# Kernel optimization log

Hardware: AMD Instinct MI355X
Metric: run time of the kernel (lower is better)

## Reference

```python
import jax, jax.numpy as jnp
import numpy as np

N_NODES = 100000
N_EDGES = 1600000
D_IN = 64
D_OUT = 64
NUM_ETYPE = 2
NEG_SLOPE = 0.2


def setup_inputs() -> dict:
    key = jax.random.key(0)
    ks = jax.random.split(key, 9)
    feat = jax.random.normal(ks[0], (N_NODES, D_IN), dtype=jnp.float32)
    rel = jax.random.uniform(ks[1], (N_EDGES, NUM_ETYPE), dtype=jnp.float32)
    W_self = jax.random.normal(ks[2], (D_OUT, D_IN), dtype=jnp.float32) * 0.1
    b_self = jax.random.normal(ks[3], (D_OUT,), dtype=jnp.float32) * 0.1
    W_neigh = jax.random.normal(ks[4], (D_OUT, D_IN), dtype=jnp.float32) * 0.1
    b_neigh = jax.random.normal(ks[5], (D_OUT,), dtype=jnp.float32) * 0.1
    attn_e = jax.random.normal(ks[6], (NUM_ETYPE, 1), dtype=jnp.float32)
    src = jax.random.randint(ks[7], (N_EDGES,), 0, N_NODES, dtype=jnp.int32)
    dst = jax.random.randint(ks[8], (N_EDGES,), 0, N_NODES, dtype=jnp.int32)
    return {"feat": feat, "rel": rel, "W_self": W_self, "b_self": b_self,
            "W_neigh": W_neigh, "b_neigh": b_neigh, "attn_e": attn_e,
            "src": src, "dst": dst}


def reference(feat, rel, W_self, b_self, W_neigh, b_neigh, attn_e, src, dst):
    n = feat.shape[0]
    # per-edge attention score: [E, num_etype] @ [num_etype, 1] -> [E]
    e = jnp.squeeze(rel @ attn_e, axis=1)
    e = jax.nn.leaky_relu(e, negative_slope=NEG_SLOPE)
    # edge_softmax: segment softmax over edges grouped by destination node
    emax = jax.ops.segment_max(e, dst, num_segments=n)          # [N]
    ex = jnp.exp(e - emax[dst])                                  # [E]
    denom = jax.ops.segment_sum(ex, dst, num_segments=n)        # [N]
    a = ex / denom[dst]                                          # [E]
    # u_mul_e + sum aggregation: neigh[v] = sum_e a_e * feat[src_e]
    m = feat[src] * a[:, None]                                   # [E, D_IN]
    h_neigh = jax.ops.segment_sum(m, dst, num_segments=n)       # [N, D_IN]
    # rst = fc_self(h_self) + fc_neigh(h_neigh)  (torch Linear: x @ W.T + b)
    return feat @ W_self.T + b_self + h_neigh @ W_neigh.T + b_neigh
```

## Files before the change

kernel.cpp:

```cpp
#include <hip/hip_runtime.h>
#include <hip/hip_bf16.h>

#define N_NODES 100000
#define N_EDGES 1600000
#define D 64
#define NEG_SLOPE 0.2f

#define BSHIFT 9
#define BNODES 512
#define NBUCK ((N_NODES + BNODES - 1) >> BSHIFT)
#define BUCKET_CAP 8896
#define P1_EPB 4096
#define P1_T 512
#define P1_IT (P1_EPB / P1_T)
#define GRID_BIN ((N_EDGES + P1_EPB - 1) / P1_EPB)

typedef __attribute__((ext_vector_type(8))) short bf16x8;
typedef __attribute__((ext_vector_type(4))) float f32x4;
#define MFMA16(a, b, c) __builtin_amdgcn_mfma_f32_16x16x32_bf16(a, b, c, 0, 0, 0)

__device__ __forceinline__ short bf16_rne(float f) {
    unsigned u = __float_as_uint(f);
    u += 0x7FFFu + ((u >> 16) & 1u);
    return (short)(u >> 16);
}
__device__ __forceinline__ float bf16_to_f(short h) {
    return __uint_as_float(((unsigned)(unsigned short)h) << 16);
}
__device__ __forceinline__ void cvt8(float4 f0, float4 f1,
                                     bf16x8& hi, bf16x8& lo) {
    float v[8] = {f0.x, f0.y, f0.z, f0.w, f1.x, f1.y, f1.z, f1.w};
    #pragma unroll
    for (int j = 0; j < 8; ++j) {
        short h = bf16_rne(v[j]);
        hi[j] = h;
        lo[j] = bf16_rne(v[j] - bf16_to_f(h));
    }
}

__global__ __launch_bounds__(P1_T) void binning_kernel(
    const float2* __restrict__ rel, const float* __restrict__ attn_e,
    const int* __restrict__ src, const int* __restrict__ dst,
    int* __restrict__ bucket_cursor, uint2* __restrict__ binned,
    const float* __restrict__ W_self, const float* __restrict__ W_neigh,
    const float* __restrict__ b_self, const float* __restrict__ b_neigh,
    bf16x8* __restrict__ wfrag, float* __restrict__ bsum)
{
    __shared__ uint2 staged1[P1_EPB];
    __shared__ uint2 staged2[P1_EPB];
    __shared__ int cnt[NBUCK];
    __shared__ int excl[NBUCK];
    __shared__ int chunkbase[NBUCK];

    int tid = threadIdx.x;

    if (blockIdx.x == GRID_BIN) {
        if (tid < D) bsum[tid] = b_self[tid] + b_neigh[tid];
        for (int c = tid; c < 1024; c += P1_T) {
            int nt = c >> 8;
            int mat = (c >> 7) & 1;
            int s = (c >> 6) & 1;
            int lane = c & 63;
            const float* Wm = mat ? W_neigh : W_self;
            int row = nt * 16 + (lane & 15);
            int koff = s * 32 + (lane >> 4) * 8;
            const float4* p = (const float4*)(Wm + row * D + koff);
            bf16x8 hi, lo;
            cvt8(p[0], p[1], hi, lo);
            int base = (c >> 6) * 128 + (c & 63);
            wfrag[base] = hi;
            wfrag[base + 64] = lo;
        }
        return;
    }

    int e0 = blockIdx.x * P1_EPB;
    int n = min(P1_EPB, N_EDGES - e0);

    for (int b = tid; b < NBUCK; b += P1_T) cnt[b] = 0;
    __syncthreads();

    float a0 = attn_e[0], a1 = attn_e[1];

    int myslot[P1_IT];
    #pragma unroll
    for (int j = 0; j < P1_IT; ++j) {
        int i = tid + j * P1_T;
        if (i < n) {
            int e = e0 + i;
            float2 r = rel[e];
            float sc = r.x * a0 + r.y * a1;
            sc = (sc > 0.f) ? sc : NEG_SLOPE * sc;
            float ev = __expf(sc);
            unsigned u = __float_as_uint(ev) + 0x8000u;
            unsigned wcode = (u >> 16) & 0x7FFFu;
            unsigned s = (unsigned)src[e];
            unsigned d = (unsigned)dst[e];
            staged1[i] = make_uint2((s << 15) | wcode, d);
            myslot[j] = atomicAdd(&cnt[d >> BSHIFT], 1);
        }
    }
    __syncthreads();
    if (tid == 0) {
        int run = 0;
        for (int b = 0; b < NBUCK; ++b) { excl[b] = run; run += cnt[b]; }
    }
    __syncthreads();
    #pragma unroll
    for (int j = 0; j < P1_IT; ++j) {
        int i = tid + j * P1_T;
        if (i < n) {
            uint2 v = staged1[i];
            staged2[excl[v.y >> BSHIFT] + myslot[j]] = v;
        }
    }
    if (tid < NBUCK)
        chunkbase[tid] = atomicAdd(&bucket_cursor[tid], cnt[tid]);
    __syncthreads();
    for (int i = tid; i < n; i += P1_T) {
        uint2 v = staged2[i];
        int b = (int)(v.y >> BSHIFT);
        binned[(size_t)b * BUCKET_CAP + chunkbase[b] + (i - excl[b])] = v;
    }
}

__global__ __launch_bounds__(1024) void csr_kernel(
    const int* __restrict__ bucket_cursor, const uint2* __restrict__ binned,
    int* __restrict__ offsets, unsigned* __restrict__ edata)
{
    __shared__ unsigned vals[BUCKET_CAP];
    __shared__ int hist[BNODES];
    __shared__ int nexcl[BNODES];
    __shared__ int cur[BNODES];
    __shared__ int bc[NBUCK];
    __shared__ int base_sh;

    int b = blockIdx.x;
    int tid = threadIdx.x;

    if (tid < NBUCK) bc[tid] = bucket_cursor[tid];
    if (tid < BNODES) { hist[tid] = 0; cur[tid] = 0; }
    __syncthreads();
    if (tid == 0) {
        int s = 0;
        for (int i = 0; i < b; ++i) s += bc[i];
        base_sh = s;
    }
    __syncthreads();
    int count = bc[b];
    int base = base_sh;
    const uint2* bin = binned + (size_t)b * BUCKET_CAP;

    for (int i = tid; i < count; i += 1024)
        atomicAdd(&hist[bin[i].y & (BNODES - 1)], 1);
    __syncthreads();

    int h = 0;
    if (tid < BNODES) { h = hist[tid]; nexcl[tid] = h; }
    __syncthreads();
    for (int d = 1; d < BNODES; d <<= 1) {
        int u = (tid >= d && tid < BNODES) ? nexcl[tid - d] : 0;
        __syncthreads();
        if (tid < BNODES) nexcl[tid] += u;
        __syncthreads();
    }
    int excl = 0;
    if (tid < BNODES) excl = nexcl[tid] - h;
    __syncthreads();
    if (tid < BNODES) nexcl[tid] = excl;
    __syncthreads();

    int node = (b << BSHIFT) + tid;
    if (tid < BNODES && node < N_NODES) offsets[node] = base + excl;
    if (b == NBUCK - 1 && tid == 0) offsets[N_NODES] = N_EDGES;

    for (int i = tid; i < count; i += 1024) {
        uint2 e = bin[i];
        int d = e.y & (BNODES - 1);
        int t = atomicAdd(&cur[d], 1);
        vals[nexcl[d] + t] = e.x;
    }
    __syncthreads();
    for (int i = tid; i < count; i += 1024)
        edata[base + i] = vals[i];
}

__global__ __launch_bounds__(256) void gemm_fused_kernel(
    const float* __restrict__ feat, const bf16x8* __restrict__ wfrag,
    const float* __restrict__ bsum, float* __restrict__ out,
    __hip_bfloat16* __restrict__ g)
{
    int tid = threadIdx.x;
    int lane = tid & 63;
    int wave = tid >> 6;
    int llo = lane & 15;
    int lhi = lane >> 4;
    int rb = blockIdx.x * 64 + wave * 16;
    if (rb >= N_NODES) return;

    int node = rb + llo;
    bool valid = node < N_NODES;
    int nclamp = valid ? node : N_NODES - 1;
    const float4* fr = (const float4*)(feat + (size_t)nclamp * D);
    bf16x8 fhi[2], flo[2];
    #pragma unroll
    for (int s = 0; s < 2; ++s)
        cvt8(fr[s * 8 + lhi * 2], fr[s * 8 + lhi * 2 + 1], fhi[s], flo[s]);

    const float4* bs4 = (const float4*)bsum;
    unsigned short* g16 = (unsigned short*)g;

    #pragma unroll
    for (int nt = 0; nt < 4; ++nt) {
        int base = nt * 512 + lane;
        bf16x8 wSh0 = wfrag[base];
        bf16x8 wSl0 = wfrag[base + 64];
        bf16x8 wSh1 = wfrag[base + 128];
        bf16x8 wSl1 = wfrag[base + 192];
        bf16x8 wNh0 = wfrag[base + 256];
        bf16x8 wNl0 = wfrag[base + 320];
        bf16x8 wNh1 = wfrag[base + 384];
        bf16x8 wNl1 = wfrag[base + 448];
        f32x4 accS = {0.f, 0.f, 0.f, 0.f};
        f32x4 accN = {0.f, 0.f, 0.f, 0.f};
        accS = MFMA16(wSh0, fhi[0], accS);
        accN = MFMA16(wNh0, fhi[0], accN);
        accS = MFMA16(wSl0, fhi[0], accS);
        accN = MFMA16(wNl0, fhi[0], accN);
        accS = MFMA16(wSh0, flo[0], accS);
        accN = MFMA16(wNh0, flo[0], accN);
        accS = MFMA16(wSh1, fhi[1], accS);
        accN = MFMA16(wNh1, fhi[1], accN);
        accS = MFMA16(wSl1, fhi[1], accS);
        accN = MFMA16(wNl1, fhi[1], accN);
        accS = MFMA16(wSh1, flo[1], accS);
        accN = MFMA16(wNh1, flo[1], accN);

        if (valid) {
            float4 bb = bs4[nt * 4 + lhi];
            float4 o;
            o.x = accS[0] + bb.x;
            o.y = accS[1] + bb.y;
            o.z = accS[2] + bb.z;
            o.w = accS[3] + bb.w;
            *(float4*)(out + (size_t)node * D + nt * 16 + lhi * 4) = o;
            uint2 gp;
            gp.x = (unsigned)(unsigned short)bf16_rne(accN[0])
                 | ((unsigned)(unsigned short)bf16_rne(accN[1]) << 16);
            gp.y = (unsigned)(unsigned short)bf16_rne(accN[2])
                 | ((unsigned)(unsigned short)bf16_rne(accN[3]) << 16);
            *(uint2*)(g16 + (size_t)node * D + nt * 16 + lhi * 4) = gp;
        }
    }
}

__global__ __launch_bounds__(256) void aggregate_kernel(
    const uint* __restrict__ g32, const unsigned* __restrict__ edata,
    const int* __restrict__ offsets, float* __restrict__ out)
{
    int v = blockIdx.x * 4 + (threadIdx.x >> 6);
    int lane = threadIdx.x & 63;
    int q = lane >> 4;
    int t = lane & 15;
    int lo = offsets[v], hi = offsets[v + 1];
    float4 acc = make_float4(0.f, 0.f, 0.f, 0.f);
    float sum = 0.f;

    for (int i = lo; i < hi; i += 16) {
        int e0 = i + q;
        int e1 = i + 4 + q;
        int e2 = i + 8 + q;
        int e3 = i + 12 + q;
        int ec0 = (e0 < hi) ? e0 : hi - 1;
        int ec1 = (e1 < hi) ? e1 : hi - 1;
        int ec2 = (e2 < hi) ? e2 : hi - 1;
        int ec3 = (e3 < hi) ? e3 : hi - 1;
        unsigned p0 = edata[ec0];
        unsigned p1 = edata[ec1];
        unsigned p2 = edata[ec2];
        unsigned p3 = edata[ec3];
        float w0 = (e0 < hi) ? __uint_as_float((p0 & 0x7FFFu) << 16) : 0.f;
        float w1 = (e1 < hi) ? __uint_as_float((p1 & 0x7FFFu) << 16) : 0.f;
        float w2 = (e2 < hi) ? __uint_as_float((p2 & 0x7FFFu) << 16) : 0.f;
        float w3 = (e3 < hi) ? __uint_as_float((p3 & 0x7FFFu) << 16) : 0.f;
        const uint2* r0 = (const uint2*)(g32 + (size_t)(p0 >> 15) * (D / 2));
        const uint2* r1 = (const uint2*)(g32 + (size_t)(p1 >> 15) * (D / 2));
        const uint2* r2 = (const uint2*)(g32 + (size_t)(p2 >> 15) * (D / 2));
        const uint2* r3 = (const uint2*)(g32 + (size_t)(p3 >> 15) * (D / 2));
        uint2 u0 = r0[t];
        uint2 u1 = r1[t];
        uint2 u2 = r2[t];
        uint2 u3 = r3[t];
        acc.x += w0 * __uint_as_float(u0.x << 16);
        acc.y += w0 * __uint_as_float(u0.x & 0xFFFF0000u);
        acc.z += w0 * __uint_as_float(u0.y << 16);
        acc.w += w0 * __uint_as_float(u0.y & 0xFFFF0000u);
        sum += w0;
        acc.x += w1 * __uint_as_float(u1.x << 16);
        acc.y += w1 * __uint_as_float(u1.x & 0xFFFF0000u);
        acc.z += w1 * __uint_as_float(u1.y << 16);
        acc.w += w1 * __uint_as_float(u1.y & 0xFFFF0000u);
        sum += w1;
        acc.x += w2 * __uint_as_float(u2.x << 16);
        acc.y += w2 * __uint_as_float(u2.x & 0xFFFF0000u);
        acc.z += w2 * __uint_as_float(u2.y << 16);
        acc.w += w2 * __uint_as_float(u2.y & 0xFFFF0000u);
        sum += w2;
        acc.x += w3 * __uint_as_float(u3.x << 16);
        acc.y += w3 * __uint_as_float(u3.x & 0xFFFF0000u);
        acc.z += w3 * __uint_as_float(u3.y << 16);
        acc.w += w3 * __uint_as_float(u3.y & 0xFFFF0000u);
        sum += w3;
    }
    #pragma unroll
    for (int mm = 16; mm <= 32; mm <<= 1) {
        acc.x += __shfl_xor(acc.x, mm, 64);
        acc.y += __shfl_xor(acc.y, mm, 64);
        acc.z += __shfl_xor(acc.z, mm, 64);
        acc.w += __shfl_xor(acc.w, mm, 64);
        sum   += __shfl_xor(sum,   mm, 64);
    }
    if (hi > lo && q == 0) {
        float inv = 1.f / sum;
        float4* orow = (float4*)(out + (size_t)v * D);
        float4 c = orow[t];
        c.x += acc.x * inv; c.y += acc.y * inv;
        c.z += acc.z * inv; c.w += acc.w * inv;
        orow[t] = c;
    }
}

extern "C" void kernel_launch(void* const* d_in, const int* in_sizes, int n_in,
                              void* d_out, int out_size, void* d_ws, size_t ws_size,
                              hipStream_t stream) {
    const float* feat    = (const float*)d_in[0];
    const float* rel     = (const float*)d_in[1];
    const float* W_self  = (const float*)d_in[2];
    const float* b_self  = (const float*)d_in[3];
    const float* W_neigh = (const float*)d_in[4];
    const float* b_neigh = (const float*)d_in[5];
    const float* attn_e  = (const float*)d_in[6];
    const int*   src     = (const int*)d_in[7];
    const int*   dst     = (const int*)d_in[8];
    float* out = (float*)d_out;

    uint2* binned = (uint2*)d_ws;
    __hip_bfloat16* g = (__hip_bfloat16*)(binned + (size_t)NBUCK * BUCKET_CAP);
    unsigned* edata = (unsigned*)((char*)g + (size_t)N_NODES * D * 2);
    bf16x8* wfrag = (bf16x8*)(edata + N_EDGES);
    float* bsum = (float*)(wfrag + 2048);
    int* offsets = (int*)(bsum + 64);
    int* bucket_cursor = offsets + N_NODES + 1;

    hipMemsetAsync(bucket_cursor, 0, NBUCK * sizeof(int), stream);

    binning_kernel<<<GRID_BIN + 1, P1_T, 0, stream>>>(
        (const float2*)rel, attn_e, src, dst, bucket_cursor, binned,
        W_self, W_neigh, b_self, b_neigh, wfrag, bsum);
    csr_kernel<<<NBUCK, 1024, 0, stream>>>(
        bucket_cursor, binned, offsets, edata);
    gemm_fused_kernel<<<(N_NODES + 63) / 64, 256, 0, stream>>>(
        feat, wfrag, bsum, out, g);
    aggregate_kernel<<<N_NODES / 4, 256, 0, stream>>>(
        (const uint*)g, edata, offsets, out);
}
```

Measured before the change: 189.8 us.

## Fuse GEMM into binning kernel, use fp16 neighbor buffer, widen aggregate loads

Merges the node GEMM into the binning launch as extra blocks that build the weight fragments in shared memory, so the separate GEMM launch and the global wfrag/bsum round trip go away and GEMM work can overlap with binning. It replaces the serial bucket prefix sums in the binning and CSR kernels with wave-shuffle scans. The projected neighbor features are now stored as fp16 instead of bf16. The aggregate kernel loads 16-byte chunks per lane with 8 edges in flight instead of 16 lanes of 8 bytes, which changes memory-level parallelism and gains mantissa precision at the risk of fp16 range overflow.

```diff
diff --git a/kernel.cpp b/kernel.cpp
--- a/kernel.cpp
+++ b/kernel.cpp
@@ -1,5 +1,6 @@
 #include <hip/hip_runtime.h>
 #include <hip/hip_bf16.h>
+#include <hip/hip_fp16.h>
 
 #define N_NODES 100000
 #define N_EDGES 1600000
@@ -14,6 +15,7 @@
 #define P1_T 512
 #define P1_IT (P1_EPB / P1_T)
 #define GRID_BIN ((N_EDGES + P1_EPB - 1) / P1_EPB)
+#define GEMM_BLKS ((N_NODES + 127) / 128)
 
 typedef __attribute__((ext_vector_type(8))) short bf16x8;
 typedef __attribute__((ext_vector_type(4))) float f32x4;
@@ -38,41 +40,107 @@
     }
 }
 
-__global__ __launch_bounds__(P1_T) void binning_kernel(
+#define SM_BYTES 67904
+
+__global__ __launch_bounds__(P1_T) void fused_bin_gemm_kernel(
     const float2* __restrict__ rel, const float* __restrict__ attn_e,
     const int* __restrict__ src, const int* __restrict__ dst,
     int* __restrict__ bucket_cursor, uint2* __restrict__ binned,
+    const float* __restrict__ feat,
     const float* __restrict__ W_self, const float* __restrict__ W_neigh,
     const float* __restrict__ b_self, const float* __restrict__ b_neigh,
-    bf16x8* __restrict__ wfrag, float* __restrict__ bsum)
+    float* __restrict__ out, __half* __restrict__ g)
 {
-    __shared__ uint2 staged1[P1_EPB];
-    __shared__ uint2 staged2[P1_EPB];
-    __shared__ int cnt[NBUCK];
-    __shared__ int excl[NBUCK];
-    __shared__ int chunkbase[NBUCK];
-
+    __shared__ __align__(16) char smem[SM_BYTES];
     int tid = threadIdx.x;
 
-    if (blockIdx.x == GRID_BIN) {
+    if (blockIdx.x >= GRID_BIN) {
+        bf16x8* wfrag = (bf16x8*)smem;
+        float* bsum = (float*)(smem + 32768);
         if (tid < D) bsum[tid] = b_self[tid] + b_neigh[tid];
         for (int c = tid; c < 1024; c += P1_T) {
             int nt = c >> 8;
             int mat = (c >> 7) & 1;
             int s = (c >> 6) & 1;
-            int lane = c & 63;
+            int ln = c & 63;
             const float* Wm = mat ? W_neigh : W_self;
-            int row = nt * 16 + (lane & 15);
-            int koff = s * 32 + (lane >> 4) * 8;
+            int row = nt * 16 + (ln & 15);
+            int koff = s * 32 + (ln >> 4) * 8;
             const float4* p = (const float4*)(Wm + row * D + koff);
             bf16x8 hi, lo;
             cvt8(p[0], p[1], hi, lo);
-            int base = (c >> 6) * 128 + (c & 63);
+            int base = (c >> 6) * 128 + ln;
             wfrag[base] = hi;
             wfrag[base + 64] = lo;
         }
+        __syncthreads();
+
+        int lane = tid & 63;
+        int wave = tid >> 6;
+        int llo = lane & 15;
+        int lhi = lane >> 4;
+        int rb = (blockIdx.x - GRID_BIN) * 128 + wave * 16;
+        if (rb >= N_NODES) return;
+
+        int node = rb + llo;
+        bool valid = node < N_NODES;
+        int nclamp = valid ? node : N_NODES - 1;
+        const float4* fr = (const float4*)(feat + (size_t)nclamp * D);
+        bf16x8 fhi[2], flo[2];
+        #pragma unroll
+        for (int s = 0; s < 2; ++s)
+            cvt8(fr[s * 8 + lhi * 2], fr[s * 8 + lhi * 2 + 1], fhi[s], flo[s]);
+
+        const float4* bs4 = (const float4*)bsum;
+        #pragma unroll
+        for (int nt = 0; nt < 4; ++nt) {
+            int base = nt * 512 + lane;
+            bf16x8 wSh0 = wfrag[base];
+            bf16x8 wSl0 = wfrag[base + 64];
+            bf16x8 wSh1 = wfrag[base + 128];
+            bf16x8 wSl1 = wfrag[base + 192];
+            bf16x8 wNh0 = wfrag[base + 256];
+            bf16x8 wNl0 = wfrag[base + 320];
+            bf16x8 wNh1 = wfrag[base + 384];
+            bf16x8 wNl1 = wfrag[base + 448];
+            f32x4 accS = {0.f, 0.f, 0.f, 0.f};
+            f32x4 accN = {0.f, 0.f, 0.f, 0.f};
+            accS = MFMA16(wSh0, fhi[0], accS);
+            accN = MFMA16(wNh0, fhi[0], accN);
+            accS = MFMA16(wSl0, fhi[0], accS);
+            accN = MFMA16(wNl0, fhi[0], accN);
+            accS = MFMA16(wSh0, flo[0], accS);
+            accN = MFMA16(wNh0, flo[0], accN);
+            accS = MFMA16(wSh1, fhi[1], accS);
+            accN = MFMA16(wNh1, fhi[1], accN);
+            accS = MFMA16(wSl1, fhi[1], accS);
+            accN = MFMA16(wNl1, fhi[1], accN);
+            accS = MFMA16(wSh1, flo[1], accS);
+            accN = MFMA16(wNh1, flo[1], accN);
+
+            if (valid) {
+                float4 bb = bs4[nt * 4 + lhi];
+                float4 o;
+                o.x = accS[0] + bb.x;
+                o.y = accS[1] + bb.y;
+                o.z = accS[2] + bb.z;
+                o.w = accS[3] + bb.w;
+                *(float4*)(out + (size_t)node * D + nt * 16 + lhi * 4) = o;
+                __half2 hA = __floats2half2_rn(accN[0], accN[1]);
+                __half2 hB = __floats2half2_rn(accN[2], accN[3]);
+                uint2 gp = make_uint2(*(unsigned*)&hA, *(unsigned*)&hB);
+                *(uint2*)(g + (size_t)node * D + nt * 16 + lhi * 4) = gp;
+            }
+        }
         return;
     }
+
+    uint2* staged1 = (uint2*)smem;
+    uint2* staged2 = (uint2*)(smem + 32768);
+    int* cnt = (int*)(smem + 65536);
+    int* excl = (int*)(smem + 65536 + 784);
+    int* chunkbase = (int*)(smem + 65536 + 1568);
+    int* wtot = (int*)(smem + 65536 + 2352);
 
     int e0 = blockIdx.x * P1_EPB;
     int n = min(P1_EPB, N_EDGES - e0);
@@ -101,11 +169,25 @@
         }
     }
     __syncthreads();
-    if (tid == 0) {
-        int run = 0;
-        for (int b = 0; b < NBUCK; ++b) { excl[b] = run; run += cnt[b]; }
-    }
-    __syncthreads();
+    {
+        int ln = tid & 63, wv = tid >> 6;
+        int c = 0;
+        if (tid < 256) c = (tid < NBUCK) ? cnt[tid] : 0;
+        int x = c;
+        #pragma unroll
+        for (int dd = 1; dd < 64; dd <<= 1) {
+            int y = __shfl_up(x, dd, 64);
+            if (ln >= dd) x += y;
+        }
+        if (tid < 256 && ln == 63) wtot[wv] = x;
+        __syncthreads();
+        if (tid < NBUCK) {
+            int wbase = 0;
+            for (int k = 0; k < wv; ++k) wbase += wtot[k];
+            excl[tid] = wbase + x - c;
+        }
+        __syncthreads();
+    }
     #pragma unroll
     for (int j = 0; j < P1_IT; ++j) {
         int i = tid + j * P1_T;
@@ -133,6 +215,7 @@
     __shared__ int nexcl[BNODES];
     __shared__ int cur[BNODES];
     __shared__ int bc[NBUCK];
+    __shared__ int wtot[8];
     __shared__ int base_sh;
 
     int b = blockIdx.x;
@@ -155,23 +238,28 @@
         atomicAdd(&hist[bin[i].y & (BNODES - 1)], 1);
     __syncthreads();
 
-    int h = 0;
-    if (tid < BNODES) { h = hist[tid]; nexcl[tid] = h; }
-    __syncthreads();
-    for (int d = 1; d < BNODES; d <<= 1) {
-        int u = (tid >= d && tid < BNODES) ? nexcl[tid - d] : 0;
-        __syncthreads();
-        if (tid < BNODES) nexcl[tid] += u;
-        __syncthreads();
-    }
-    int excl = 0;
-    if (tid < BNODES) excl = nexcl[tid] - h;
-    __syncthreads();
-    if (tid < BNODES) nexcl[tid] = excl;
-    __syncthreads();
+    {
+        int ln = tid & 63, wv = tid >> 6;
+        int h = 0;
+        if (tid < BNODES) h = hist[tid];
+        int x = h;
+        #pragma unroll
+        for (int dd = 1; dd < 64; dd <<= 1) {
+            int y = __shfl_up(x, dd, 64);
+            if (ln >= dd) x += y;
+        }
+        if (tid < BNODES && ln == 63) wtot[wv] = x;
+        __syncthreads();
+        if (tid < BNODES) {
+            int wbase = 0;
+            for (int k = 0; k < wv; ++k) wbase += wtot[k];
+            nexcl[tid] = wbase + x - h;
+        }
+        __syncthreads();
+    }
 
     int node = (b << BSHIFT) + tid;
-    if (tid < BNODES && node < N_NODES) offsets[node] = base + excl;
+    if (tid < BNODES && node < N_NODES) offsets[node] = base + nexcl[tid];
     if (b == NBUCK - 1 && tid == 0) offsets[N_NODES] = N_EDGES;
 
     for (int i = tid; i < count; i += 1024) {
@@ -185,148 +273,80 @@
         edata[base + i] = vals[i];
 }
 
-__global__ __launch_bounds__(256) void gemm_fused_kernel(
-    const float* __restrict__ feat, const bf16x8* __restrict__ wfrag,
-    const float* __restrict__ bsum, float* __restrict__ out,
-    __hip_bfloat16* __restrict__ g)
-{
-    int tid = threadIdx.x;
-    int lane = tid & 63;
-    int wave = tid >> 6;
-    int llo = lane & 15;
-    int lhi = lane >> 4;
-    int rb = blockIdx.x * 64 + wave * 16;
-    if (rb >= N_NODES) return;
-
-    int node = rb + llo;
-    bool valid = node < N_NODES;
-    int nclamp = valid ? node : N_NODES - 1;
-    const float4* fr = (const float4*)(feat + (size_t)nclamp * D);
-    bf16x8 fhi[2], flo[2];
-    #pragma unroll
-    for (int s = 0; s < 2; ++s)
-        cvt8(fr[s * 8 + lhi * 2], fr[s * 8 + lhi * 2 + 1], fhi[s], flo[s]);
-
-    const float4* bs4 = (const float4*)bsum;
-    unsigned short* g16 = (unsigned short*)g;
-
-    #pragma unroll
-    for (int nt = 0; nt < 4; ++nt) {
-        int base = nt * 512 + lane;
-        bf16x8 wSh0 = wfrag[base];
-        bf16x8 wSl0 = wfrag[base + 64];
-        bf16x8 wSh1 = wfrag[base + 128];
-        bf16x8 wSl1 = wfrag[base + 192];
-        bf16x8 wNh0 = wfrag[base + 256];
-        bf16x8 wNl0 = wfrag[base + 320];
-        bf16x8 wNh1 = wfrag[base + 384];
-        bf16x8 wNl1 = wfrag[base + 448];
-        f32x4 accS = {0.f, 0.f, 0.f, 0.f};
-        f32x4 accN = {0.f, 0.f, 0.f, 0.f};
-        accS = MFMA16(wSh0, fhi[0], accS);
-        accN = MFMA16(wNh0, fhi[0], accN);
-        accS = MFMA16(wSl0, fhi[0], accS);
-        accN = MFMA16(wNl0, fhi[0], accN);
-        accS = MFMA16(wSh0, flo[0], accS);
-        accN = MFMA16(wNh0, flo[0], accN);
-        accS = MFMA16(wSh1, fhi[1], accS);
-        accN = MFMA16(wNh1, fhi[1], accN);
-        accS = MFMA16(wSl1, fhi[1], accS);
-        accN = MFMA16(wNl1, fhi[1], accN);
-        accS = MFMA16(wSh1, flo[1], accS);
-        accN = MFMA16(wNh1, flo[1], accN);
-
-        if (valid) {
-            float4 bb = bs4[nt * 4 + lhi];
-            float4 o;
-            o.x = accS[0] + bb.x;
-            o.y = accS[1] + bb.y;
-            o.z = accS[2] + bb.z;
-            o.w = accS[3] + bb.w;
-            *(float4*)(out + (size_t)node * D + nt * 16 + lhi * 4) = o;
-            uint2 gp;
-            gp.x = (unsigned)(unsigned short)bf16_rne(accN[0])
-                 | ((unsigned)(unsigned short)bf16_rne(accN[1]) << 16);
-            gp.y = (unsigned)(unsigned short)bf16_rne(accN[2])
-                 | ((unsigned)(unsigned short)bf16_rne(accN[3]) << 16);
-            *(uint2*)(g16 + (size_t)node * D + nt * 16 + lhi * 4) = gp;
-        }
-    }
-}
-
 __global__ __launch_bounds__(256) void aggregate_kernel(
-    const uint* __restrict__ g32, const unsigned* __restrict__ edata,
+    const __half* __restrict__ g, const unsigned* __restrict__ edata,
     const int* __restrict__ offsets, float* __restrict__ out)
 {
     int v = blockIdx.x * 4 + (threadIdx.x >> 6);
     int lane = threadIdx.x & 63;
-    int q = lane >> 4;
-    int t = lane & 15;
+    int q = lane >> 3;
+    int t = lane & 7;
     int lo = offsets[v], hi = offsets[v + 1];
-    float4 acc = make_float4(0.f, 0.f, 0.f, 0.f);
+    float4 acc0 = make_float4(0.f, 0.f, 0.f, 0.f);
+    float4 acc1 = make_float4(0.f, 0.f, 0.f, 0.f);
     float sum = 0.f;
 
     for (int i = lo; i < hi; i += 16) {
         int e0 = i + q;
-        int e1 = i + 4 + q;
-        int e2 = i + 8 + q;
-        int e3 = i + 12 + q;
+        int e1 = i + 8 + q;
         int ec0 = (e0 < hi) ? e0 : hi - 1;
         int ec1 = (e1 < hi) ? e1 : hi - 1;
-        int ec2 = (e2 < hi) ? e2 : hi - 1;
-        int ec3 = (e3 < hi) ? e3 : hi - 1;
         unsigned p0 = edata[ec0];
         unsigned p1 = edata[ec1];
-        unsigned p2 = edata[ec2];
-        unsigned p3 = edata[ec3];
         float w0 = (e0 < hi) ? __uint_as_float((p0 & 0x7FFFu) << 16) : 0.f;
         float w1 = (e1 < hi) ? __uint_as_float((p1 & 0x7FFFu) << 16) : 0.f;
-        float w2 = (e2 < hi) ? __uint_as_float((p2 & 0x7FFFu) << 16) : 0.f;
-        float w3 = (e3 < hi) ? __uint_as_float((p3 & 0x7FFFu) << 16) : 0.f;
-        const uint2* r0 = (const uint2*)(g32 + (size_t)(p0 >> 15) * (D / 2));
-        const uint2* r1 = (const uint2*)(g32 + (size_t)(p1 >> 15) * (D / 2));
-        const uint2* r2 = (const uint2*)(g32 + (size_t)(p2 >> 15) * (D / 2));
-        const uint2* r3 = (const uint2*)(g32 + (size_t)(p3 >> 15) * (D / 2));
-        uint2 u0 = r0[t];
-        uint2 u1 = r1[t];
-        uint2 u2 = r2[t];
-        uint2 u3 = r3[t];
-        acc.x += w0 * __uint_as_float(u0.x << 16);
-        acc.y += w0 * __uint_as_float(u0.x & 0xFFFF0000u);
-        acc.z += w0 * __uint_as_float(u0.y << 16);
-        acc.w += w0 * __uint_as_float(u0.y & 0xFFFF0000u);
-        sum += w0;
-        acc.x += w1 * __uint_as_float(u1.x << 16);
-        acc.y += w1 * __uint_as_float(u1.x & 0xFFFF0000u);
-        acc.z += w1 * __uint_as_float(u1.y << 16);
-        acc.w += w1 * __uint_as_float(u1.y & 0xFFFF0000u);
-        sum += w1;
-        acc.x += w2 * __uint_as_float(u2.x << 16);
-        acc.y += w2 * __uint_as_float(u2.x & 0xFFFF0000u);
-        acc.z += w2 * __uint_as_float(u2.y << 16);
-        acc.w += w2 * __uint_as_float(u2.y & 0xFFFF0000u);
-        sum += w2;
-        acc.x += w3 * __uint_as_float(u3.x << 16);
-        acc.y += w3 * __uint_as_float(u3.x & 0xFFFF0000u);
-        acc.z += w3 * __uint_as_float(u3.y << 16);
-        acc.w += w3 * __uint_as_float(u3.y & 0xFFFF0000u);
-        sum += w3;
+        const uint4* r0 = (const uint4*)(g + (size_t)(p0 >> 15) * D);
+        const uint4* r1 = (const uint4*)(g + (size_t)(p1 >> 15) * D);
+        uint4 u0 = r0[t];
+        uint4 u1 = r1[t];
+        {
+            float2 f;
+            f = __half22float2(*(const __half2*)&u0.x);
+            acc0.x = fmaf(w0, f.x, acc0.x); acc0.y = fmaf(w0, f.y, acc0.y);
+            f = __half22float2(*(const __half2*)&u0.y);
+            acc0.z = fmaf(w0, f.x, acc0.z); acc0.w = fmaf(w0, f.y, acc0.w);
+            f = __half22float2(*(const __half2*)&u0.z);
+            acc1.x = fmaf(w0, f.x, acc1.x); acc1.y = fmaf(w0, f.y, acc1.y);
+            f = __half22float2(*(const __half2*)&u0.w);
+            acc1.z = fmaf(w0, f.x, acc1.z); acc1.w = fmaf(w0, f.y, acc1.w);
+            sum += w0;
+        }
+        {
+            float2 f;
+            f = __half22float2(*(const __half2*)&u1.x);
+            acc0.x = fmaf(w1, f.x, acc0.x); acc0.y = fmaf(w1, f.y, acc0.y);
+            f = __half22float2(*(const __half2*)&u1.y);
+            acc0.z = fmaf(w1, f.x, acc0.z); acc0.w = fmaf(w1, f.y, acc0.w);
+            f = __half22float2(*(const __half2*)&u1.z);
+            acc1.x = fmaf(w1, f.x, acc1.x); acc1.y = fmaf(w1, f.y, acc1.y);
+            f = __half22float2(*(const __half2*)&u1.w);
+            acc1.z = fmaf(w1, f.x, acc1.z); acc1.w = fmaf(w1, f.y, acc1.w);
+            sum += w1;
+        }
     }
     #pragma unroll
-    for (int mm = 16; mm <= 32; mm <<= 1) {
-        acc.x += __shfl_xor(acc.x, mm, 64);
-        acc.y += __shfl_xor(acc.y, mm, 64);
-        acc.z += __shfl_xor(acc.z, mm, 64);
-        acc.w += __shfl_xor(acc.w, mm, 64);
+    for (int mm = 8; mm <= 32; mm <<= 1) {
+        acc0.x += __shfl_xor(acc0.x, mm, 64);
+        acc0.y += __shfl_xor(acc0.y, mm, 64);
+        acc0.z += __shfl_xor(acc0.z, mm, 64);
+        acc0.w += __shfl_xor(acc0.w, mm, 64);
+        acc1.x += __shfl_xor(acc1.x, mm, 64);
+        acc1.y += __shfl_xor(acc1.y, mm, 64);
+        acc1.z += __shfl_xor(acc1.z, mm, 64);
+        acc1.w += __shfl_xor(acc1.w, mm, 64);
         sum   += __shfl_xor(sum,   mm, 64);
     }
     if (hi > lo && q == 0) {
         float inv = 1.f / sum;
         float4* orow = (float4*)(out + (size_t)v * D);
-        float4 c = orow[t];
-        c.x += acc.x * inv; c.y += acc.y * inv;
-        c.z += acc.z * inv; c.w += acc.w * inv;
-        orow[t] = c;
+        float4 c0 = orow[2 * t];
+        float4 c1 = orow[2 * t + 1];
+        c0.x += acc0.x * inv; c0.y += acc0.y * inv;
+        c0.z += acc0.z * inv; c0.w += acc0.w * inv;
+        c1.x += acc1.x * inv; c1.y += acc1.y * inv;
+        c1.z += acc1.z * inv; c1.w += acc1.w * inv;
+        orow[2 * t] = c0;
+        orow[2 * t + 1] = c1;
     }
 }
 
@@ -345,22 +365,18 @@
     float* out = (float*)d_out;
 
     uint2* binned = (uint2*)d_ws;
-    __hip_bfloat16* g = (__hip_bfloat16*)(binned + (size_t)NBUCK * BUCKET_CAP);
+    __half* g = (__half*)(binned + (size_t)NBUCK * BUCKET_CAP);
     unsigned* edata = (unsigned*)((char*)g + (size_t)N_NODES * D * 2);
-    bf16x8* wfrag = (bf16x8*)(edata + N_EDGES);
-    float* bsum = (float*)(wfrag + 2048);
-    int* offsets = (int*)(bsum + 64);
+    int* offsets = (int*)(edata + N_EDGES);
     int* bucket_cursor = offsets + N_NODES + 1;
 
     hipMemsetAsync(bucket_cursor, 0, NBUCK * sizeof(int), stream);
 
-    binning_kernel<<<GRID_BIN + 1, P1_T, 0, stream>>>(
+    fused_bin_gemm_kernel<<<GRID_BIN + GEMM_BLKS, P1_T, 0, stream>>>(
         (const float2*)rel, attn_e, src, dst, bucket_cursor, binned,
-        W_self, W_neigh, b_self, b_neigh, wfrag, bsum);
+        feat, W_self, W_neigh, b_self, b_neigh, out, g);
     csr_kernel<<<NBUCK, 1024, 0, stream>>>(
         bucket_cursor, binned, offsets, edata);
-    gemm_fused_kernel<<<(N_NODES + 63) / 64, 256, 0, stream>>>(
-        feat, wfrag, bsum, out, g);
     aggregate_kernel<<<N_NODES / 4, 256, 0, stream>>>(
-        (const uint*)g, edata, offsets, out);
-}
+        g, edata, offsets, out);
+}
```

Result: faster. 177.8 us (-6.3%).
